# Kernel tuning notes

Hardware: AMD Instinct MI355X
Metric: run time of the kernel (lower is better)

The kernel has to match this reference:

```python
import jax, jax.numpy as jnp
import numpy as np

N_PRED = 29
F_DIM = 8192
H1 = 256
H2 = 128


def setup_inputs() -> dict:
    key = jax.random.key(0)
    ks = jax.random.split(key, 7)
    features = jax.random.normal(ks[0], (4096, F_DIM), dtype=jnp.float32)
    # Stacked per-predicate MLP weights (PyTorch Linear init scale ~ 1/sqrt(fan_in))
    W1 = jax.random.normal(ks[1], (N_PRED, F_DIM, H1), dtype=jnp.float32) / np.sqrt(F_DIM)
    b1 = jax.random.normal(ks[2], (N_PRED, H1), dtype=jnp.float32) / np.sqrt(F_DIM)
    W2 = jax.random.normal(ks[3], (N_PRED, H1, H2), dtype=jnp.float32) / np.sqrt(H1)
    b2 = jax.random.normal(ks[4], (N_PRED, H2), dtype=jnp.float32) / np.sqrt(H1)
    W3 = jax.random.normal(ks[5], (N_PRED, H2), dtype=jnp.float32) / np.sqrt(H2)
    b3 = jax.random.normal(ks[6], (N_PRED,), dtype=jnp.float32) / np.sqrt(H2)
    return {"features": features, "W1": W1, "b1": b1, "W2": W2, "b2": b2, "W3": W3, "b3": b3}


def reference(features, W1, b1, W2, b2, W3, b3):
    # 29 parallel heads as one batched (grouped) GEMM chain; dropout = identity (eval).
    h1 = jax.nn.relu(jnp.einsum('bf,pfh->bph', features, W1) + b1[None])   # [B, P, H1]
    h2 = jax.nn.relu(jnp.einsum('bph,phk->bpk', h1, W2) + b2[None])        # [B, P, H2]
    logits = jnp.einsum('bpk,pk->bp', h2, W3) + b3[None]                   # [B, P]
    return jax.nn.sigmoid(logits)
```

## Files before the change

### kernel.cpp

```cpp
#include <hip/hip_runtime.h>
#include <hip/hip_bf16.h>

typedef __attribute__((ext_vector_type(8))) short short8_t;
typedef __attribute__((ext_vector_type(8))) __bf16 bf16x8;
typedef __attribute__((ext_vector_type(4))) float f32x4;

__device__ __forceinline__ void gload16(const void* g, void* l) {
  __builtin_amdgcn_global_load_lds(
      (const __attribute__((address_space(1))) void*)g,
      (__attribute__((address_space(3))) void*)l, 16, 0, 0);
}

__device__ __forceinline__ unsigned short f2bf(float f) {
  __hip_bfloat16 h = __float2bfloat16(f);
  return __builtin_bit_cast(unsigned short, h);
}


__global__ void k_cvt_feat(const float* __restrict__ in, unsigned short* __restrict__ out) {
  const size_t N = (size_t)4096 * 8192;
  size_t i = ((size_t)blockIdx.x * 256 + threadIdx.x) * 4;
  const size_t stride = (size_t)gridDim.x * 256 * 4;
  for (; i < N; i += stride) {
    float4 v = *(const float4*)(in + i);
    ushort4 o;
    o.x = f2bf(v.x); o.y = f2bf(v.y); o.z = f2bf(v.z); o.w = f2bf(v.w);
    *(ushort4*)(out + i) = o;
  }
}

__global__ void k_cvt_w1(const float* __restrict__ W1, unsigned short* __restrict__ out, int p0) {
  __shared__ unsigned short t[64][66];
  const int p = p0 + blockIdx.z;
  const float* src = W1 + (size_t)p * 8192 * 256;
  unsigned short* dst = out + (size_t)blockIdx.z * 256 * 8192;
  const int f0 = blockIdx.x * 64, h0 = blockIdx.y * 64;
#pragma unroll
  for (int i = 0; i < 16; ++i) {
    int tt = i * 256 + threadIdx.x;
    int r = tt >> 6, c = tt & 63;
    t[r][c] = f2bf(src[(size_t)(f0 + r) * 256 + h0 + c]);
  }
  __syncthreads();
#pragma unroll
  for (int i = 0; i < 16; ++i) {
    int tt = i * 256 + threadIdx.x;
    int r = tt >> 6, c = tt & 63;
    dst[(size_t)(h0 + r) * 8192 + f0 + c] = t[c][r];
  }
}

__global__ void k_cvt_w2(const float* __restrict__ W2, unsigned short* __restrict__ out) {
  const int p = blockIdx.x;
  const float* src = W2 + (size_t)p * 256 * 128;
  unsigned short* dst = out + (size_t)p * 128 * 256;
  for (int tt = threadIdx.x; tt < 128 * 256; tt += 256) {
    int j = tt >> 8, h = tt & 255;
    dst[tt] = f2bf(src[(size_t)h * 128 + j]);
  }
}

__global__ __launch_bounds__(256, 2) void k_gemm1(
    const unsigned short* __restrict__ A,
    const unsigned short* __restrict__ Bt,
    const float* __restrict__ b1,
    unsigned short* __restrict__ h1,
    int p0) {
  __shared__ __align__(16) unsigned short lds_a[128 * 64];
  __shared__ __align__(16) unsigned short lds_b[128 * 64];
  const int tid = threadIdx.x;
  const int lane = tid & 63;
  const int wave = tid >> 6;
  const int m0 = blockIdx.x * 128;
  const int n0 = blockIdx.y * 128;
  const int z = blockIdx.z;
  const int p = p0 + z;
  const int wr = wave >> 1, wc = wave & 1;

  const unsigned short* Ab = A + (size_t)m0 * 8192;
  const unsigned short* Bb = Bt + ((size_t)z * 256 + n0) * 8192;

  const unsigned short* gA[4];
  const unsigned short* gB[4];
  unsigned short* lA[4];
  unsigned short* lB[4];
#pragma unroll
  for (int i = 0; i < 4; ++i) {
    int t = i * 256 + tid;
    int r = t >> 3;
    int uu = (t & 7) ^ (r & 7);
    gA[i] = Ab + (size_t)r * 8192 + uu * 8;
    gB[i] = Bb + (size_t)r * 8192 + uu * 8;
    int lb = (i * 256 + wave * 64) * 8;
    lA[i] = &lds_a[lb];
    lB[i] = &lds_b[lb];
  }

  f32x4 acc[4][4] = {};

  for (int k0 = 0; k0 < 8192; k0 += 64) {
    __syncthreads();
#pragma unroll
    for (int i = 0; i < 4; ++i) {
      gload16(gA[i] + k0, lA[i]);
      gload16(gB[i] + k0, lB[i]);
    }
    __syncthreads();
#pragma unroll
    for (int kk = 0; kk < 64; kk += 32) {
      const int ku = (kk >> 3) + (lane >> 4);
      bf16x8 af[4], bfv[4];
#pragma unroll
      for (int mi = 0; mi < 4; ++mi) {
        int row = wr * 64 + mi * 16 + (lane & 15);
        int u = ku ^ (row & 7);
        af[mi] = __builtin_bit_cast(bf16x8, *(const short8_t*)&lds_a[row * 64 + u * 8]);
      }
#pragma unroll
      for (int nj = 0; nj < 4; ++nj) {
        int row = wc * 64 + nj * 16 + (lane & 15);
        int u = ku ^ (row & 7);
        bfv[nj] = __builtin_bit_cast(bf16x8, *(const short8_t*)&lds_b[row * 64 + u * 8]);
      }
#pragma unroll
      for (int mi = 0; mi < 4; ++mi)
#pragma unroll
        for (int nj = 0; nj < 4; ++nj)
          acc[mi][nj] = __builtin_amdgcn_mfma_f32_16x16x32_bf16(af[mi], bfv[nj], acc[mi][nj], 0, 0, 0);
    }
  }

  const int col16 = lane & 15, rg = lane >> 4;
#pragma unroll
  for (int nj = 0; nj < 4; ++nj) {
    const int col = n0 + wc * 64 + nj * 16 + col16;
    const float bb = b1[p * 256 + col];
#pragma unroll
    for (int mi = 0; mi < 4; ++mi) {
      const int mbase = m0 + wr * 64 + mi * 16 + rg * 4;
#pragma unroll
      for (int r = 0; r < 4; ++r) {
        float v = acc[mi][nj][r] + bb;
        v = v > 0.f ? v : 0.f;
        h1[((size_t)p * 4096 + mbase + r) * 256 + col] = f2bf(v);
      }
    }
  }
}

__global__ __launch_bounds__(256, 2) void k_gemm23(
    const unsigned short* __restrict__ h1,
    const unsigned short* __restrict__ W2t,
    const float* __restrict__ b2,
    const float* __restrict__ W3,
    const float* __restrict__ b3,
    float* __restrict__ out) {
  __shared__ __align__(16) unsigned short lds_a[128 * 64];
  __shared__ __align__(16) unsigned short lds_b[128 * 64];
  const int tid = threadIdx.x;
  const int lane = tid & 63;
  const int wave = tid >> 6;
  const int m0 = blockIdx.x * 128;
  const int p = blockIdx.y;

  const unsigned short* Ab = h1 + ((size_t)p * 4096 + m0) * 256;
  const unsigned short* Bb = W2t + (size_t)p * 128 * 256;

  f32x4 acc[2][8] = {};

  for (int k0 = 0; k0 < 256; k0 += 64) {
    __syncthreads();
#pragma unroll
    for (int i = 0; i < 4; ++i) {
      int t = i * 256 + tid;
      int r = t >> 3;
      int uu = (t & 7) ^ (r & 7);
      gload16(Ab + (size_t)r * 256 + k0 + uu * 8, &lds_a[(i * 256 + wave * 64) * 8]);
      gload16(Bb + (size_t)r * 256 + k0 + uu * 8, &lds_b[(i * 256 + wave * 64) * 8]);
    }
    __syncthreads();
#pragma unroll
    for (int kk = 0; kk < 64; kk += 32) {
      const int ku = (kk >> 3) + (lane >> 4);
      bf16x8 af[2], bfv[8];
#pragma unroll
      for (int mi = 0; mi < 2; ++mi) {
        int row = wave * 32 + mi * 16 + (lane & 15);
        int u = ku ^ (row & 7);
        af[mi] = __builtin_bit_cast(bf16x8, *(const short8_t*)&lds_a[row * 64 + u * 8]);
      }
#pragma unroll
      for (int nj = 0; nj < 8; ++nj) {
        int row = nj * 16 + (lane & 15);
        int u = ku ^ (row & 7);
        bfv[nj] = __builtin_bit_cast(bf16x8, *(const short8_t*)&lds_b[row * 64 + u * 8]);
      }
#pragma unroll
      for (int mi = 0; mi < 2; ++mi)
#pragma unroll
        for (int nj = 0; nj < 8; ++nj)
          acc[mi][nj] = __builtin_amdgcn_mfma_f32_16x16x32_bf16(af[mi], bfv[nj], acc[mi][nj], 0, 0, 0);
    }
  }

  float b2v[8], w3v[8];
  const int c16 = lane & 15;
#pragma unroll
  for (int nj = 0; nj < 8; ++nj) {
    int c = nj * 16 + c16;
    b2v[nj] = b2[p * 128 + c];
    w3v[nj] = W3[p * 128 + c];
  }
  const float b3p = b3[p];
#pragma unroll
  for (int mi = 0; mi < 2; ++mi) {
#pragma unroll
    for (int r = 0; r < 4; ++r) {
      float s = 0.f;
#pragma unroll
      for (int nj = 0; nj < 8; ++nj) {
        float v = acc[mi][nj][r] + b2v[nj];
        v = v > 0.f ? v : 0.f;
        s += v * w3v[nj];
      }
      s += __shfl_xor(s, 1);
      s += __shfl_xor(s, 2);
      s += __shfl_xor(s, 4);
      s += __shfl_xor(s, 8);
      if ((lane & 15) == 0) {
        int m = m0 + wave * 32 + mi * 16 + (lane >> 4) * 4 + r;
        float logit = s + b3p;
        out[(size_t)m * 29 + p] = 1.f / (1.f + __expf(-logit));
      }
    }
  }
}

extern "C" void kernel_launch(void* const* d_in, const int* in_sizes, int n_in,
                              void* d_out, int out_size, void* d_ws, size_t ws_size,
                              hipStream_t stream) {
  const float* features = (const float*)d_in[0];
  const float* W1 = (const float*)d_in[1];
  const float* b1 = (const float*)d_in[2];
  const float* W2 = (const float*)d_in[3];
  const float* b2 = (const float*)d_in[4];
  const float* W3 = (const float*)d_in[5];
  const float* b3 = (const float*)d_in[6];
  float* out = (float*)d_out;

  char* ws = (char*)d_ws;
  const size_t featB = (size_t)4096 * 8192 * 2;
  const size_t h1B   = (size_t)29 * 4096 * 256 * 2;
  const size_t w2B   = (size_t)29 * 128 * 256 * 2;
  const size_t w1pp  = (size_t)256 * 8192 * 2;

  unsigned short* featbf = (unsigned short*)ws;
  unsigned short* h1bf   = (unsigned short*)(ws + featB);
  unsigned short* w2t    = (unsigned short*)(ws + featB + h1B);
  unsigned short* w1t    = (unsigned short*)(ws + featB + h1B + w2B);

  size_t base = featB + h1B + w2B;
  size_t rem = (ws_size > base) ? (ws_size - base) : 0;
  int CH = (int)(rem / w1pp);
  if (CH > 29) CH = 29;
  if (CH < 1) CH = 1;

  k_cvt_feat<<<2048, 256, 0, stream>>>(features, featbf);
  k_cvt_w2<<<29, 256, 0, stream>>>(W2, w2t);

  for (int p0 = 0; p0 < 29; p0 += CH) {
    int c = (29 - p0) < CH ? (29 - p0) : CH;
    k_cvt_w1<<<dim3(128, 4, c), 256, 0, stream>>>(W1, w1t, p0);
    k_gemm1<<<dim3(32, 2, c), 256, 0, stream>>>(featbf, w1t, b1, h1bf, p0);
  }

  k_gemm23<<<dim3(32, 29), 256, 0, stream>>>(h1bf, w2t, b2, W3, b3, out);
}
```

Baseline: 611.6 us.

## Rewrite gemm1 as 256x256-tile, 4-stage pipelined MFMA kernel with XCD remap

The first grouped GEMM now uses 512-thread blocks computing 256x256 output tiles, with a 4-buffer LDS ring and loads issued three K-steps ahead. It splits each K-step into two MFMA halves separated by barriers, with s_setprio and explicit vmcnt waits. Workgroup IDs are remapped so that consecutive tiles land on the same XCD. The goal is to hide global-load latency, raise arithmetic intensity per block, and improve L2 locality, at the cost of much more LDS (128KB), more registers, and fewer blocks in flight.

```diff
diff --git a/kernel.cpp b/kernel.cpp
--- a/kernel.cpp
+++ b/kernel.cpp
@@ -60,89 +60,132 @@
   }
 }
 
-__global__ __launch_bounds__(256, 2) void k_gemm1(
+__global__ __launch_bounds__(512, 2) void k_gemm1(
     const unsigned short* __restrict__ A,
     const unsigned short* __restrict__ Bt,
     const float* __restrict__ b1,
     unsigned short* __restrict__ h1,
     int p0) {
-  __shared__ __align__(16) unsigned short lds_a[128 * 64];
-  __shared__ __align__(16) unsigned short lds_b[128 * 64];
+  __shared__ __align__(16) unsigned short SA[4 * 8192];
+  __shared__ __align__(16) unsigned short SB[4 * 8192];
+
   const int tid = threadIdx.x;
   const int lane = tid & 63;
   const int wave = tid >> 6;
-  const int m0 = blockIdx.x * 128;
-  const int n0 = blockIdx.y * 128;
-  const int z = blockIdx.z;
+  const int wm = wave >> 2;
+  const int wn = wave & 3;
+
+  const int nwg = gridDim.x * gridDim.y;
+  const int orig = blockIdx.y * gridDim.x + blockIdx.x;
+  const int q = nwg >> 3, r_ = nwg & 7;
+  const int xcd = orig & 7, idx = orig >> 3;
+  const int wg = (xcd < r_ ? xcd * (q + 1) : r_ * (q + 1) + (xcd - r_) * q) + idx;
+  const int mx = wg & 15;
+  const int z = wg >> 4;
   const int p = p0 + z;
-  const int wr = wave >> 1, wc = wave & 1;
+  const int m0 = mx * 256;
 
   const unsigned short* Ab = A + (size_t)m0 * 8192;
-  const unsigned short* Bb = Bt + ((size_t)z * 256 + n0) * 8192;
-
-  const unsigned short* gA[4];
-  const unsigned short* gB[4];
-  unsigned short* lA[4];
-  unsigned short* lB[4];
-#pragma unroll
-  for (int i = 0; i < 4; ++i) {
-    int t = i * 256 + tid;
-    int r = t >> 3;
-    int uu = (t & 7) ^ (r & 7);
-    gA[i] = Ab + (size_t)r * 8192 + uu * 8;
-    gB[i] = Bb + (size_t)r * 8192 + uu * 8;
-    int lb = (i * 256 + wave * 64) * 8;
-    lA[i] = &lds_a[lb];
-    lB[i] = &lds_b[lb];
-  }
-
-  f32x4 acc[4][4] = {};
-
-  for (int k0 = 0; k0 < 8192; k0 += 64) {
-    __syncthreads();
-#pragma unroll
-    for (int i = 0; i < 4; ++i) {
-      gload16(gA[i] + k0, lA[i]);
-      gload16(gB[i] + k0, lB[i]);
-    }
-    __syncthreads();
-#pragma unroll
-    for (int kk = 0; kk < 64; kk += 32) {
-      const int ku = (kk >> 3) + (lane >> 4);
-      bf16x8 af[4], bfv[4];
-#pragma unroll
-      for (int mi = 0; mi < 4; ++mi) {
-        int row = wr * 64 + mi * 16 + (lane & 15);
-        int u = ku ^ (row & 7);
-        af[mi] = __builtin_bit_cast(bf16x8, *(const short8_t*)&lds_a[row * 64 + u * 8]);
-      }
-#pragma unroll
-      for (int nj = 0; nj < 4; ++nj) {
-        int row = wc * 64 + nj * 16 + (lane & 15);
-        int u = ku ^ (row & 7);
-        bfv[nj] = __builtin_bit_cast(bf16x8, *(const short8_t*)&lds_b[row * 64 + u * 8]);
-      }
-#pragma unroll
-      for (int mi = 0; mi < 4; ++mi)
-#pragma unroll
-        for (int nj = 0; nj < 4; ++nj)
-          acc[mi][nj] = __builtin_amdgcn_mfma_f32_16x16x32_bf16(af[mi], bfv[nj], acc[mi][nj], 0, 0, 0);
-    }
-  }
-
-  const int col16 = lane & 15, rg = lane >> 4;
+  const unsigned short* Bb = Bt + (size_t)z * 256 * 8192;
+
+  const unsigned short* pA0; const unsigned short* pA1;
+  const unsigned short* pB0; const unsigned short* pB1;
+  {
+    int e0 = tid,        r0 = e0 >> 2, u0 = (e0 & 3) ^ ((r0 >> 1) & 3);
+    int e1 = 512 + tid,  r1 = e1 >> 2, u1 = (e1 & 3) ^ ((r1 >> 1) & 3);
+    pA0 = Ab + (size_t)r0 * 8192 + u0 * 8;
+    pA1 = Ab + (size_t)r1 * 8192 + u1 * 8;
+    pB0 = Bb + (size_t)r0 * 8192 + u0 * 8;
+    pB1 = Bb + (size_t)r1 * 8192 + u1 * 8;
+  }
+  const int lao0 = (wave * 64) * 8;
+  const int lao1 = (512 + wave * 64) * 8;
+
+  const int arow = wm * 128 + (lane & 15);
+  const int brow = wn * 64 + (lane & 15);
+  const int a_off0 = arow * 32 + ((((arow >> 1) & 3) ^ (lane >> 4)) * 8);
+  const int b_off0 = brow * 32 + ((((brow >> 1) & 3) ^ (lane >> 4)) * 8);
+
+  f32x4 acc[8][4] = {};
+
+  const int NT = 8192 / 32;
+
+  auto stageA = [&](int T) {
+    const int k0 = T * 32, cb = T & 3;
+    gload16(pA0 + k0, SA + cb * 8192 + lao0);
+    gload16(pA1 + k0, SA + cb * 8192 + lao1);
+  };
+  auto stageB = [&](int T) {
+    const int k0 = T * 32, cb = T & 3;
+    gload16(pB0 + k0, SB + cb * 8192 + lao0);
+    gload16(pB1 + k0, SB + cb * 8192 + lao1);
+  };
+
+  auto kstep = [&](int T, bool PF, int VM) {
+    const int cb = T & 3;
+    const unsigned short* sa = SA + cb * 8192;
+    const unsigned short* sb = SB + cb * 8192;
+    bf16x8 bfr[4], afr[4];
+#pragma unroll
+    for (int nj = 0; nj < 4; ++nj) bfr[nj] = __builtin_bit_cast(bf16x8, *(const short8_t*)(sb + b_off0 + nj * 512));
+#pragma unroll
+    for (int mi = 0; mi < 4; ++mi) afr[mi] = __builtin_bit_cast(bf16x8, *(const short8_t*)(sa + a_off0 + mi * 512));
+    if (PF) stageA(T + 3);
+    __builtin_amdgcn_s_barrier();
+    asm volatile("s_waitcnt lgkmcnt(0)" ::: "memory");
+    __builtin_amdgcn_sched_barrier(0);
+    __builtin_amdgcn_s_setprio(1);
+#pragma unroll
+    for (int mi = 0; mi < 4; ++mi)
+#pragma unroll
+      for (int nj = 0; nj < 4; ++nj)
+        acc[mi][nj] = __builtin_amdgcn_mfma_f32_16x16x32_bf16(afr[mi], bfr[nj], acc[mi][nj], 0, 0, 0);
+    __builtin_amdgcn_s_setprio(0);
+    __builtin_amdgcn_s_barrier();
+    __builtin_amdgcn_sched_barrier(0);
+#pragma unroll
+    for (int mi = 0; mi < 4; ++mi) afr[mi] = __builtin_bit_cast(bf16x8, *(const short8_t*)(sa + a_off0 + (mi + 4) * 512));
+    if (PF) stageB(T + 3);
+    __builtin_amdgcn_s_barrier();
+    asm volatile("s_waitcnt lgkmcnt(0)" ::: "memory");
+    __builtin_amdgcn_sched_barrier(0);
+    __builtin_amdgcn_s_setprio(1);
+#pragma unroll
+    for (int mi = 0; mi < 4; ++mi)
+#pragma unroll
+      for (int nj = 0; nj < 4; ++nj)
+        acc[mi + 4][nj] = __builtin_amdgcn_mfma_f32_16x16x32_bf16(afr[mi], bfr[nj], acc[mi + 4][nj], 0, 0, 0);
+    __builtin_amdgcn_s_setprio(0);
+    if (VM == 8)      asm volatile("s_waitcnt vmcnt(8)" ::: "memory");
+    else if (VM == 4) asm volatile("s_waitcnt vmcnt(4)" ::: "memory");
+    else if (VM == 0) asm volatile("s_waitcnt vmcnt(0)" ::: "memory");
+    __builtin_amdgcn_s_barrier();
+    __builtin_amdgcn_sched_barrier(0);
+  };
+
+  stageA(0); stageB(0); stageA(1); stageB(1); stageA(2); stageB(2);
+  asm volatile("s_waitcnt vmcnt(8)" ::: "memory");
+  __builtin_amdgcn_s_barrier();
+  __builtin_amdgcn_sched_barrier(0);
+
+  for (int t = 0; t < NT - 3; ++t) kstep(t, true, 8);
+  kstep(NT - 3, false, 4);
+  kstep(NT - 2, false, 0);
+  kstep(NT - 1, false, -1);
+
+  const int rg = lane >> 4, c16 = lane & 15;
 #pragma unroll
   for (int nj = 0; nj < 4; ++nj) {
-    const int col = n0 + wc * 64 + nj * 16 + col16;
+    const int col = wn * 64 + nj * 16 + c16;
     const float bb = b1[p * 256 + col];
 #pragma unroll
-    for (int mi = 0; mi < 4; ++mi) {
-      const int mbase = m0 + wr * 64 + mi * 16 + rg * 4;
-#pragma unroll
-      for (int r = 0; r < 4; ++r) {
-        float v = acc[mi][nj][r] + bb;
+    for (int mi = 0; mi < 8; ++mi) {
+      const int rbase = m0 + wm * 128 + mi * 16 + rg * 4;
+#pragma unroll
+      for (int rr = 0; rr < 4; ++rr) {
+        float v = acc[mi][nj][rr] + bb;
         v = v > 0.f ? v : 0.f;
-        h1[((size_t)p * 4096 + mbase + r) * 256 + col] = f2bf(v);
+        h1[((size_t)p * 4096 + rbase + rr) * 256 + col] = f2bf(v);
       }
     }
   }
@@ -271,7 +314,7 @@
   for (int p0 = 0; p0 < 29; p0 += CH) {
     int c = (29 - p0) < CH ? (29 - p0) : CH;
     k_cvt_w1<<<dim3(128, 4, c), 256, 0, stream>>>(W1, w1t, p0);
-    k_gemm1<<<dim3(32, 2, c), 256, 0, stream>>>(featbf, w1t, b1, h1bf, p0);
+    k_gemm1<<<dim3(16, c), 512, 0, stream>>>(featbf, w1t, b1, h1bf, p0);
   }
 
   k_gemm23<<<dim3(32, 29), 256, 0, stream>>>(h1bf, w2t, b2, W3, b3, out);
```

Result: slower. 852.4 us (+39.4%).
